# Performance work log

Measured on AMD Instinct MI355X. Metric: run time of the kernel, lower is better.

The kernel has to match this reference:

```python
import jax, jax.numpy as jnp
import numpy as np

B, N, C, H = 2, 2048, 1024, 16
D = C // H
SCALE = 1.0 / np.sqrt(D)
MASK_VAL = -10000.0


def setup_inputs() -> dict:
    key = jax.random.key(0)
    k1, k2, k3 = jax.random.split(key, 3)
    hidden_state = jax.random.normal(k1, (B, N, C), dtype=jnp.float32)
    attention_mask = jax.random.randint(k2, (B, N), 0, 2) == 1  # True = padded
    # fused QKV projection weight, torch Linear convention: y = x @ W.T, W: [3C, C]
    W = jax.random.normal(k3, (3 * C, C), dtype=jnp.float32) * 0.02
    return {"hidden_state": hidden_state, "W": W, "attention_mask": attention_mask}


def reference(hidden_state, W, attention_mask):
    b, n, c = hidden_state.shape
    # fused QKV: [B,N,3C] -> [B,N,3,H,D] -> [3,B,H,N,D]
    wx = jnp.einsum('bnc,oc->bno', hidden_state, W).reshape(b, n, 3, H, D)
    wx = jnp.transpose(wx, (2, 0, 3, 1, 4))
    q, k, v = wx[0], wx[1], wx[2]
    scores = jnp.einsum('bhid,bhjd->bhij', q, k) * SCALE
    # construct_mask: pairwise OR of per-token padding mask, broadcast over heads
    m = attention_mask
    expanded = (m[:, None, :, None] | m[:, None, None, :])  # [B,1,N,N]
    scores = jnp.where(expanded, MASK_VAL, scores)
    scores = scores - jnp.max(scores, axis=-1, keepdims=True)
    att_weights = jax.nn.softmax(scores, axis=-1)
    # dropout_rate = 0.0 -> identity
    att = jnp.einsum('bhij,bhjd->bhid', att_weights, v)
    att = jnp.transpose(att, (0, 2, 1, 3)).reshape(b, n, c)
    return (att, att_weights)
```

## Files before the change

kernel.cpp:

```cpp
#include <hip/hip_runtime.h>


typedef unsigned short u16;
typedef __attribute__((ext_vector_type(8))) short bf16x8;
typedef __attribute__((ext_vector_type(4))) float f32x4;

#define B_ 2
#define N_ 2048
#define H_ 16
#define D_ 64
#define QKV_MAT 4194304
#define ATTW_OFF 4194304
#define SCALE_ 0.125f
#define OFF_MASK 25165824
#define OFF_FLAG 25182208
#define OFF_XB   25182464
#define OFF_WB   33571072

__device__ __forceinline__ u16 f32_bf16(float f) {
  unsigned u = __float_as_uint(f);
  u += 0x7fffu + ((u >> 16) & 1u);
  return (u16)(u >> 16);
}
__device__ __forceinline__ float bf16_f32(unsigned h) {
  return __uint_as_float(h << 16);
}
__device__ __forceinline__ bf16x8 ld_frag(const u16* p) { return *(const bf16x8*)p; }
__device__ __forceinline__ void cp16(u16* l, const u16* g) { *(bf16x8*)l = *(const bf16x8*)g; }

__global__ void detect_prep(const unsigned char* __restrict__ mraw,
                            const unsigned* __restrict__ X32,
                            int* __restrict__ mout, int* __restrict__ flag) {
  __shared__ int votes, mflags;
  const int tid = threadIdx.x;
  if (tid == 0) { votes = 0; mflags = 0; }
  __syncthreads();
  int v = 0;
  for (int i = tid; i < 4096; i += 256) {
    unsigned low = X32[i] & 0xFFFFu;
    unsigned e = (low >> 7) & 0xFFu;
    if (low == 0 || (e >= 80 && e <= 150)) v++;
  }
  atomicAdd(&votes, v);
  int fl = 0;
  for (int p = tid; p < B_ * N_; p += 256) {
    unsigned char c = mraw[p];
    if (c > 1) fl |= 1;
    if (c && (p & 3) == 1) fl |= 4;
    if (c && (p & 3) != 0) fl |= 2;
    if (c && (p & 7) == 4) fl |= 8;
  }
  if (fl) atomicOr(&mflags, fl);
  __syncthreads();
  const int f = mflags;
  if (tid == 0) flag[0] = (votes < 2600) ? 1 : 0;
  for (int i = tid; i < B_ * N_; i += 256) {
    int m;
    if (f & 1) {
      if (f & 4) m = (((const u16*)mraw)[i] & 0x7FFFu) != 0;
      else       m = (((const unsigned*)mraw)[i] << 1) != 0;
    } else if (f & 2) m = mraw[i] != 0;
    else if (f & 8)   m = ((const int*)mraw)[i] != 0;
    else              m = ((const long long*)mraw)[i] != 0;
    mout[i] = m;
  }
}

__global__ __launch_bounds__(256) void convert_in(const void* __restrict__ X,
                                                  const void* __restrict__ W,
                                                  u16* __restrict__ Xb, u16* __restrict__ Wb,
                                                  const int* __restrict__ flag) {
  const int f32m = flag[0];
  const int XC = (B_ * N_ * 1024) / 8;
  const int WC = (3072 * 1024) / 8;
  for (int idx = blockIdx.x * 256 + threadIdx.x; idx < XC + WC; idx += gridDim.x * 256) {
    const void* src; u16* dst; int c;
    if (idx < XC) { c = idx; src = X; dst = Xb; }
    else          { c = idx - XC; src = W; dst = Wb; }
    if (f32m) {
      const float4* s = (const float4*)src;
      float4 a = s[c * 2], b = s[c * 2 + 1];
      unsigned p0 = (unsigned)f32_bf16(a.x) | ((unsigned)f32_bf16(a.y) << 16);
      unsigned p1 = (unsigned)f32_bf16(a.z) | ((unsigned)f32_bf16(a.w) << 16);
      unsigned p2 = (unsigned)f32_bf16(b.x) | ((unsigned)f32_bf16(b.y) << 16);
      unsigned p3 = (unsigned)f32_bf16(b.z) | ((unsigned)f32_bf16(b.w) << 16);
      ((uint4*)dst)[c] = make_uint4(p0, p1, p2, p3);
    } else {
      ((uint4*)dst)[c] = ((const uint4*)src)[c];
    }
  }
}

__global__ __launch_bounds__(256) void qkv_gemm(const u16* __restrict__ X,
                                                const u16* __restrict__ W,
                                                u16* __restrict__ qkv) {
  __shared__ u16 xs[128 * 64];
  __shared__ u16 wsh[128 * 64];
  const int tid = threadIdx.x;
  const int w = tid >> 6, l = tid & 63, quad = l >> 4, ln = l & 15;
  const int r0 = blockIdx.y * 128;
  const int o0 = blockIdx.x * 128;

  const f32x4 z4 = {0.f, 0.f, 0.f, 0.f};
  f32x4 acc[2][8];
#pragma unroll
  for (int rt = 0; rt < 2; rt++)
#pragma unroll
    for (int ct = 0; ct < 8; ct++) acc[rt][ct] = z4;

  for (int kc = 0; kc < 1024; kc += 64) {
#pragma unroll
    for (int ro = 0; ro < 4; ro++) {
      int q = ro * 256 + tid;
      int r = q >> 3, s = q & 7;
      int c = s ^ (r & 7);
      cp16(xs + q * 8, X + (size_t)(r0 + r) * 1024 + kc + c * 8);
      cp16(wsh + q * 8, W + (size_t)(o0 + r) * 1024 + kc + c * 8);
    }
    __syncthreads();
#pragma unroll
    for (int k2 = 0; k2 < 2; k2++) {
      bf16x8 af[2], bfr[8];
#pragma unroll
      for (int rt = 0; rt < 2; rt++) {
        int row = w * 32 + rt * 16 + ln;
        int slot = (k2 * 4 + quad) ^ (row & 7);
        af[rt] = ld_frag(xs + row * 64 + slot * 8);
      }
#pragma unroll
      for (int ct = 0; ct < 8; ct++) {
        int row = ct * 16 + ln;
        int slot = (k2 * 4 + quad) ^ (row & 7);
        bfr[ct] = ld_frag(wsh + row * 64 + slot * 8);
      }
#pragma unroll
      for (int rt = 0; rt < 2; rt++)
#pragma unroll
        for (int ct = 0; ct < 8; ct++)
          acc[rt][ct] = __builtin_amdgcn_mfma_f32_16x16x32_bf16(af[rt], bfr[ct], acc[rt][ct], 0, 0, 0);
    }
    __syncthreads();
  }

  const int b = r0 >> 11;
#pragma unroll
  for (int rt = 0; rt < 2; rt++) {
#pragma unroll
    for (int ct = 0; ct < 8; ct++) {
      int o = o0 + ct * 16 + ln;
      int sel = o >> 10;
      int h = (o >> 6) & 15;
      int d = o & 63;
      int nbase = (r0 & 2047) + w * 32 + rt * 16 + quad * 4;
      if (sel < 2) {
        size_t base = (size_t)sel * QKV_MAT + ((size_t)(b * 16 + h) * N_ + nbase) * D_ + d;
#pragma unroll
        for (int g = 0; g < 4; g++)
          qkv[base + (size_t)g * D_] = f32_bf16(acc[rt][ct][g]);
      } else {
        size_t base = 2 * (size_t)QKV_MAT + ((size_t)(b * 16 + h) * D_ + d) * N_ + nbase;
        unsigned lo = (unsigned)f32_bf16(acc[rt][ct][0]) | ((unsigned)f32_bf16(acc[rt][ct][1]) << 16);
        unsigned hi = (unsigned)f32_bf16(acc[rt][ct][2]) | ((unsigned)f32_bf16(acc[rt][ct][3]) << 16);
        *(uint2*)(qkv + base) = make_uint2(lo, hi);
      }
    }
  }
}

__global__ __launch_bounds__(256) void attn_kernel(const u16* __restrict__ qkv,
                                                   const int* __restrict__ mask,
                                                   void* __restrict__ outv,
                                                   const int* __restrict__ flag) {
  __shared__ u16 qs[128 * 64];
  __shared__ u16 ks[64 * 64];
  __shared__ u16 vs[64 * 64];
  __shared__ u16 ps[128 * 72];
  __shared__ float mrow[128];
  __shared__ float rlrow[128];

  const int of32 = flag[0];
  u16* outh = (u16*)outv;
  float* outf = (float*)outv;

  const int tid = threadIdx.x;
  const int w = tid >> 6, l = tid & 63, quad = l >> 4, ln = l & 15;
  const int bh = blockIdx.x & 31;
  const int qt = blockIdx.x >> 5;
  const int b = bh >> 4, h = bh & 15;
  const int q0 = qt * 128;

  const u16* Qg = qkv + ((size_t)bh * N_ + q0) * D_;
  const u16* Kg = qkv + QKV_MAT + (size_t)bh * N_ * D_;
  const u16* Vg = qkv + 2 * (size_t)QKV_MAT + (size_t)bh * D_ * N_;
  const int* mb = mask + b * N_;
  const size_t attw_base = (size_t)ATTW_OFF + (size_t)bh * N_ * N_ + (size_t)q0 * N_;

#pragma unroll
  for (int ro = 0; ro < 4; ro++) {
    int q = ro * 256 + tid;
    int r = q >> 3, s = q & 7;
    int c = s ^ (r & 7);
    cp16(qs + q * 8, Qg + (size_t)r * D_ + c * 8);
  }
  int rowpad[2][4];
#pragma unroll
  for (int rt = 0; rt < 2; rt++)
#pragma unroll
    for (int g = 0; g < 4; g++)
      rowpad[rt][g] = mb[q0 + w * 32 + rt * 16 + quad * 4 + g];
  __syncthreads();

  bf16x8 qa[2][2];
#pragma unroll
  for (int rt = 0; rt < 2; rt++)
#pragma unroll
    for (int k2 = 0; k2 < 2; k2++) {
      int row = w * 32 + rt * 16 + ln;
      int slot = (k2 * 4 + quad) ^ (row & 7);
      qa[rt][k2] = ld_frag(qs + row * 64 + slot * 8);
    }

  float lsum[2][4] = {{0.f, 0.f, 0.f, 0.f}, {0.f, 0.f, 0.f, 0.f}};
  const f32x4 z4 = {0.f, 0.f, 0.f, 0.f};

  for (int kt = 0; kt < 32; kt++) {
#pragma unroll
    for (int ro = 0; ro < 2; ro++) {
      int q = ro * 256 + tid;
      int r = q >> 3, s = q & 7;
      int c = s ^ (r & 7);
      cp16(ks + q * 8, Kg + (size_t)(kt * 64 + r) * D_ + c * 8);
    }
    int cp[4];
#pragma unroll
    for (int ct = 0; ct < 4; ct++) cp[ct] = mb[kt * 64 + ct * 16 + ln];
    __syncthreads();

    f32x4 sacc[2][4];
#pragma unroll
    for (int rt = 0; rt < 2; rt++)
#pragma unroll
      for (int ct = 0; ct < 4; ct++) sacc[rt][ct] = z4;
#pragma unroll
    for (int k2 = 0; k2 < 2; k2++) {
      bf16x8 kb[4];
#pragma unroll
      for (int ct = 0; ct < 4; ct++) {
        int row = ct * 16 + ln;
        int slot = (k2 * 4 + quad) ^ (row & 7);
        kb[ct] = ld_frag(ks + row * 64 + slot * 8);
      }
#pragma unroll
      for (int rt = 0; rt < 2; rt++)
#pragma unroll
        for (int ct = 0; ct < 4; ct++)
          sacc[rt][ct] = __builtin_amdgcn_mfma_f32_16x16x32_bf16(qa[rt][k2], kb[ct], sacc[rt][ct], 0, 0, 0);
    }
    __syncthreads();
#pragma unroll
    for (int rt = 0; rt < 2; rt++)
#pragma unroll
      for (int g = 0; g < 4; g++) {
        float e = 0.f;
#pragma unroll
        for (int ct = 0; ct < 4; ct++) {
          float sv = sacc[rt][ct][g] * SCALE_;
          sv = (rowpad[rt][g] | cp[ct]) ? -10000.f : sv;
          e += __expf(sv);
        }
        lsum[rt][g] += e;
      }
  }

#pragma unroll
  for (int rt = 0; rt < 2; rt++)
#pragma unroll
    for (int g = 0; g < 4; g++) {
      float lv = lsum[rt][g];
      lv += __shfl_xor(lv, 1);
      lv += __shfl_xor(lv, 2);
      lv += __shfl_xor(lv, 4);
      lv += __shfl_xor(lv, 8);
      if (ln == 0) {
        int i = w * 32 + rt * 16 + quad * 4 + g;
        mrow[i] = rowpad[rt][g] ? -10000.f : 0.f;
        rlrow[i] = rowpad[rt][g] ? (1.f / 2048.f) : (1.f / lv);
      }
    }
  __syncthreads();

  bf16x8 qb[8][2];
  float mi[8], rli[8];
#pragma unroll
  for (int it = 0; it < 8; it++) {
    int row = it * 16 + ln;
#pragma unroll
    for (int k2 = 0; k2 < 2; k2++) {
      int slot = (k2 * 4 + quad) ^ (row & 7);
      qb[it][k2] = ld_frag(qs + row * 64 + slot * 8);
    }
    mi[it] = mrow[row];
    rli[it] = rlrow[row];
  }

  f32x4 oacc[2][4];
#pragma unroll
  for (int rt = 0; rt < 2; rt++)
#pragma unroll
    for (int dt = 0; dt < 4; dt++) oacc[rt][dt] = z4;

  for (int kt = 0; kt < 32; kt++) {
    __syncthreads();
#pragma unroll
    for (int ro = 0; ro < 2; ro++) {
      int q = ro * 256 + tid;
      int r = q >> 3, s = q & 7;
      int c = s ^ (r & 7);
      cp16(ks + q * 8, Kg + (size_t)(kt * 64 + r) * D_ + c * 8);
      cp16(vs + q * 8, Vg + (size_t)r * N_ + kt * 64 + c * 8);
    }
    int cpj[4];
#pragma unroll
    for (int g = 0; g < 4; g++) cpj[g] = mb[kt * 64 + w * 16 + quad * 4 + g];
    __syncthreads();

    bf16x8 ka[2];
#pragma unroll
    for (int k2 = 0; k2 < 2; k2++) {
      int row = w * 16 + ln;
      int slot = (k2 * 4 + quad) ^ (row & 7);
      ka[k2] = ld_frag(ks + row * 64 + slot * 8);
    }
#pragma unroll
    for (int it = 0; it < 8; it++) {
      f32x4 st = z4;
      st = __builtin_amdgcn_mfma_f32_16x16x32_bf16(ka[0], qb[it][0], st, 0, 0, 0);
      st = __builtin_amdgcn_mfma_f32_16x16x32_bf16(ka[1], qb[it][1], st, 0, 0, 0);
      bool rp = mi[it] < -5000.f;
      unsigned pk[4];
#pragma unroll
      for (int g = 0; g < 4; g++) {
        float sv = st[g] * SCALE_;
        sv = (cpj[g] || rp) ? -10000.f : sv;
        float p = __expf(sv - mi[it]) * rli[it];
        pk[g] = f32_bf16(p);
      }
      int iRow = it * 16 + ln;
      int jc = w * 16 + quad * 4;
      *(uint2*)(ps + iRow * 72 + jc) = make_uint2(pk[0] | (pk[1] << 16), pk[2] | (pk[3] << 16));
    }
    __syncthreads();

    if (!of32) {
#pragma unroll
      for (int ro = 0; ro < 4; ro++) {
        int q = ro * 256 + tid;
        int r = q >> 3, c = q & 7;
        uint4 v = *(const uint4*)(ps + r * 72 + c * 8);
        *(uint4*)(outh + attw_base + (size_t)r * N_ + kt * 64 + c * 8) = v;
      }
    } else {
#pragma unroll
      for (int ro = 0; ro < 8; ro++) {
        int q = ro * 256 + tid;
        int r = q >> 4, c4 = q & 15;
        uint2 v = *(const uint2*)(ps + r * 72 + c4 * 4);
        float4 o = make_float4(bf16_f32(v.x & 0xFFFFu), bf16_f32(v.x >> 16),
                               bf16_f32(v.y & 0xFFFFu), bf16_f32(v.y >> 16));
        *(float4*)(outf + attw_base + (size_t)r * N_ + kt * 64 + c4 * 4) = o;
      }
    }
#pragma unroll
    for (int k2 = 0; k2 < 2; k2++) {
      bf16x8 pa[2], vb[4];
#pragma unroll
      for (int rt = 0; rt < 2; rt++) {
        int row = w * 32 + rt * 16 + ln;
        pa[rt] = ld_frag(ps + row * 72 + k2 * 32 + quad * 8);
      }
#pragma unroll
      for (int dt = 0; dt < 4; dt++) {
        int row = dt * 16 + ln;
        int slot = (k2 * 4 + quad) ^ (row & 7);
        vb[dt] = ld_frag(vs + row * 64 + slot * 8);
      }
#pragma unroll
      for (int rt = 0; rt < 2; rt++)
#pragma unroll
        for (int dt = 0; dt < 4; dt++)
          oacc[rt][dt] = __builtin_amdgcn_mfma_f32_16x16x32_bf16(pa[rt], vb[dt], oacc[rt][dt], 0, 0, 0);
    }
  }

#pragma unroll
  for (int rt = 0; rt < 2; rt++)
#pragma unroll
    for (int dt = 0; dt < 4; dt++) {
      int d = dt * 16 + ln;
#pragma unroll
      for (int g = 0; g < 4; g++) {
        int i = w * 32 + rt * 16 + quad * 4 + g;
        size_t off = (size_t)(b * N_ + q0 + i) * 1024 + h * 64 + d;
        if (!of32) outh[off] = f32_bf16(oacc[rt][dt][g]);
        else       outf[off] = oacc[rt][dt][g];
      }
    }
}

extern "C" void kernel_launch(void* const* d_in, const int* in_sizes, int n_in,
                              void* d_out, int out_size, void* d_ws, size_t ws_size,
                              hipStream_t stream) {
  (void)in_sizes; (void)n_in; (void)out_size; (void)ws_size;
  const unsigned char* mraw = (const unsigned char*)d_in[2];
  char* ws = (char*)d_ws;
  u16* qkvws = (u16*)ws;
  int* maskws = (int*)(ws + OFF_MASK);
  int* flagws = (int*)(ws + OFF_FLAG);
  u16* Xb = (u16*)(ws + OFF_XB);
  u16* Wb = (u16*)(ws + OFF_WB);

  detect_prep<<<1, 256, 0, stream>>>(mraw, (const unsigned*)d_in[0], maskws, flagws);
  convert_in<<<1792, 256, 0, stream>>>(d_in[0], d_in[1], Xb, Wb, flagws);
  qkv_gemm<<<dim3(24, 32), 256, 0, stream>>>(Xb, Wb, qkvws);
  attn_kernel<<<512, 256, 0, stream>>>(qkvws, maskws, d_out, flagws);
}
```

Baseline: 700.0 us.

## Load tiles with global_load_lds, use exp2 softmax, merge mask prep into convert

Global-to-shared tile copies in the QKV GEMM and attention kernel now use direct global-to-LDS loads, so data no longer passes through VGPRs. The softmax now uses a hardware exp2 with the scale and mask value pre-multiplied by log2(e), which removes the multiply hidden inside __expf. The per-token mask conversion moves out of the single-block detect kernel into the grid-wide convert kernel, with the mask flags passed through the workspace. The direct LDS loads depend on the compiler waiting on the vector-memory counter before each barrier, and the swizzled per-lane destinations must stay contiguous per wave.

```diff
diff --git a/kernel.cpp b/kernel.cpp
--- a/kernel.cpp
+++ b/kernel.cpp
@@ -11,12 +11,14 @@
 #define D_ 64
 #define QKV_MAT 4194304
 #define ATTW_OFF 4194304
-#define SCALE_ 0.125f
 #define OFF_MASK 25165824
 #define OFF_FLAG 25182208
 #define OFF_XB   25182464
 #define OFF_WB   33571072
 
+#define SCALE_L2 0.18033688011112042f
+#define MASK_L2  -14426.950408889634f
+
 __device__ __forceinline__ u16 f32_bf16(float f) {
   unsigned u = __float_as_uint(f);
   u += 0x7fffu + ((u >> 16) & 1u);
@@ -26,11 +28,16 @@
   return __uint_as_float(h << 16);
 }
 __device__ __forceinline__ bf16x8 ld_frag(const u16* p) { return *(const bf16x8*)p; }
-__device__ __forceinline__ void cp16(u16* l, const u16* g) { *(bf16x8*)l = *(const bf16x8*)g; }
+
+__device__ __forceinline__ void gld16(u16* l, const u16* g) {
+  __builtin_amdgcn_global_load_lds(
+      (const __attribute__((address_space(1))) void*)g,
+      (__attribute__((address_space(3))) void*)l, 16, 0, 0);
+}
 
 __global__ void detect_prep(const unsigned char* __restrict__ mraw,
                             const unsigned* __restrict__ X32,
-                            int* __restrict__ mout, int* __restrict__ flag) {
+                            int* __restrict__ flag) {
   __shared__ int votes, mflags;
   const int tid = threadIdx.x;
   if (tid == 0) { votes = 0; mflags = 0; }
@@ -52,9 +59,19 @@
   }
   if (fl) atomicOr(&mflags, fl);
   __syncthreads();
-  const int f = mflags;
-  if (tid == 0) flag[0] = (votes < 2600) ? 1 : 0;
-  for (int i = tid; i < B_ * N_; i += 256) {
+  if (tid == 0) { flag[0] = (votes < 2600) ? 1 : 0; flag[1] = mflags; }
+}
+
+__global__ __launch_bounds__(256) void convert_in(const void* __restrict__ X,
+                                                  const void* __restrict__ W,
+                                                  const unsigned char* __restrict__ mraw,
+                                                  u16* __restrict__ Xb, u16* __restrict__ Wb,
+                                                  int* __restrict__ mout,
+                                                  const int* __restrict__ flag) {
+  const int f32m = flag[0];
+  const int f = flag[1];
+  const int gid = blockIdx.x * 256 + threadIdx.x;
+  for (int i = gid; i < B_ * N_; i += gridDim.x * 256) {
     int m;
     if (f & 1) {
       if (f & 4) m = (((const u16*)mraw)[i] & 0x7FFFu) != 0;
@@ -64,16 +81,9 @@
     else              m = ((const long long*)mraw)[i] != 0;
     mout[i] = m;
   }
-}
-
-__global__ __launch_bounds__(256) void convert_in(const void* __restrict__ X,
-                                                  const void* __restrict__ W,
-                                                  u16* __restrict__ Xb, u16* __restrict__ Wb,
-                                                  const int* __restrict__ flag) {
-  const int f32m = flag[0];
   const int XC = (B_ * N_ * 1024) / 8;
   const int WC = (3072 * 1024) / 8;
-  for (int idx = blockIdx.x * 256 + threadIdx.x; idx < XC + WC; idx += gridDim.x * 256) {
+  for (int idx = gid; idx < XC + WC; idx += gridDim.x * 256) {
     const void* src; u16* dst; int c;
     if (idx < XC) { c = idx; src = X; dst = Xb; }
     else          { c = idx - XC; src = W; dst = Wb; }
@@ -114,8 +124,8 @@
       int q = ro * 256 + tid;
       int r = q >> 3, s = q & 7;
       int c = s ^ (r & 7);
-      cp16(xs + q * 8, X + (size_t)(r0 + r) * 1024 + kc + c * 8);
-      cp16(wsh + q * 8, W + (size_t)(o0 + r) * 1024 + kc + c * 8);
+      gld16(xs + q * 8, X + (size_t)(r0 + r) * 1024 + kc + c * 8);
+      gld16(wsh + q * 8, W + (size_t)(o0 + r) * 1024 + kc + c * 8);
     }
     __syncthreads();
 #pragma unroll
@@ -200,7 +210,7 @@
     int q = ro * 256 + tid;
     int r = q >> 3, s = q & 7;
     int c = s ^ (r & 7);
-    cp16(qs + q * 8, Qg + (size_t)r * D_ + c * 8);
+    gld16(qs + q * 8, Qg + (size_t)r * D_ + c * 8);
   }
   int rowpad[2][4];
 #pragma unroll
@@ -229,7 +239,7 @@
       int q = ro * 256 + tid;
       int r = q >> 3, s = q & 7;
       int c = s ^ (r & 7);
-      cp16(ks + q * 8, Kg + (size_t)(kt * 64 + r) * D_ + c * 8);
+      gld16(ks + q * 8, Kg + (size_t)(kt * 64 + r) * D_ + c * 8);
     }
     int cp[4];
 #pragma unroll
@@ -264,9 +274,9 @@
         float e = 0.f;
 #pragma unroll
         for (int ct = 0; ct < 4; ct++) {
-          float sv = sacc[rt][ct][g] * SCALE_;
-          sv = (rowpad[rt][g] | cp[ct]) ? -10000.f : sv;
-          e += __expf(sv);
+          float sv = sacc[rt][ct][g] * SCALE_L2;
+          sv = (rowpad[rt][g] | cp[ct]) ? MASK_L2 : sv;
+          e += __builtin_amdgcn_exp2f(sv);
         }
         lsum[rt][g] += e;
       }
@@ -283,7 +293,7 @@
       lv += __shfl_xor(lv, 8);
       if (ln == 0) {
         int i = w * 32 + rt * 16 + quad * 4 + g;
-        mrow[i] = rowpad[rt][g] ? -10000.f : 0.f;
+        mrow[i] = rowpad[rt][g] ? MASK_L2 : 0.f;
         rlrow[i] = rowpad[rt][g] ? (1.f / 2048.f) : (1.f / lv);
       }
     }
@@ -316,8 +326,8 @@
       int q = ro * 256 + tid;
       int r = q >> 3, s = q & 7;
       int c = s ^ (r & 7);
-      cp16(ks + q * 8, Kg + (size_t)(kt * 64 + r) * D_ + c * 8);
-      cp16(vs + q * 8, Vg + (size_t)r * N_ + kt * 64 + c * 8);
+      gld16(ks + q * 8, Kg + (size_t)(kt * 64 + r) * D_ + c * 8);
+      gld16(vs + q * 8, Vg + (size_t)r * N_ + kt * 64 + c * 8);
     }
     int cpj[4];
 #pragma unroll
@@ -340,9 +350,9 @@
       unsigned pk[4];
 #pragma unroll
       for (int g = 0; g < 4; g++) {
-        float sv = st[g] * SCALE_;
-        sv = (cpj[g] || rp) ? -10000.f : sv;
-        float p = __expf(sv - mi[it]) * rli[it];
+        float sv = st[g] * SCALE_L2;
+        sv = (cpj[g] || rp) ? MASK_L2 : sv;
+        float p = __builtin_amdgcn_exp2f(sv - mi[it]) * rli[it];
         pk[g] = f32_bf16(p);
       }
       int iRow = it * 16 + ln;
@@ -419,8 +429,8 @@
   u16* Xb = (u16*)(ws + OFF_XB);
   u16* Wb = (u16*)(ws + OFF_WB);
 
-  detect_prep<<<1, 256, 0, stream>>>(mraw, (const unsigned*)d_in[0], maskws, flagws);
-  convert_in<<<1792, 256, 0, stream>>>(d_in[0], d_in[1], Xb, Wb, flagws);
+  detect_prep<<<1, 256, 0, stream>>>(mraw, (const unsigned*)d_in[0], flagws);
+  convert_in<<<1792, 256, 0, stream>>>(d_in[0], d_in[1], mraw, Xb, Wb, maskws, flagws);
   qkv_gemm<<<dim3(24, 32), 256, 0, stream>>>(Xb, Wb, qkvws);
   attn_kernel<<<512, 256, 0, stream>>>(qkvws, maskws, d_out, flagws);
 }
```

Result: no change. 713.4 us (+1.9%).
